# Kernel tuning notes

Measured on AMD Instinct MI355X. Metric: run time of the kernel, lower is better.

The kernel has to match this reference:

```python
import jax, jax.numpy as jnp
import numpy as np

V, E, T_MAX, H, L = 20000, 384, 512, 8, 8
D = E // H  # head size 48
FF = 4 * E


def setup_inputs() -> dict:
    key = jax.random.key(0)
    ks = jax.random.split(key, 24)
    B, T = 16, 512
    s = 0.02
    return {
        "index": jax.random.randint(ks[0], (B, T), 0, V, dtype=jnp.int64),
        "targets": jax.random.randint(ks[1], (B, T), 0, V, dtype=jnp.int64),
        "tok_emb": s * jax.random.normal(ks[2], (V, E), jnp.float32),
        "pos_emb": s * jax.random.normal(ks[3], (T_MAX, E), jnp.float32),
        "Wq": s * jax.random.normal(ks[4], (L, E, H, D), jnp.float32),
        "bq": jnp.zeros((L, H, D), jnp.float32),
        "Wk": s * jax.random.normal(ks[5], (L, E, H, D), jnp.float32),
        "bk": jnp.zeros((L, H, D), jnp.float32),
        "Wv": s * jax.random.normal(ks[6], (L, E, H, D), jnp.float32),
        "bv": jnp.zeros((L, H, D), jnp.float32),
        "Wo": s * jax.random.normal(ks[7], (L, E, E), jnp.float32),
        "bo": jnp.zeros((L, E), jnp.float32),
        "ln1_g": jnp.ones((L, E), jnp.float32),
        "ln1_b": jnp.zeros((L, E), jnp.float32),
        "ln2_g": jnp.ones((L, E), jnp.float32),
        "ln2_b": jnp.zeros((L, E), jnp.float32),
        "W1": s * jax.random.normal(ks[8], (L, E, FF), jnp.float32),
        "b1": jnp.zeros((L, FF), jnp.float32),
        "W2": s * jax.random.normal(ks[9], (L, FF, E), jnp.float32),
        "b2": jnp.zeros((L, E), jnp.float32),
        "lnf_g": jnp.ones((E,), jnp.float32),
        "lnf_b": jnp.zeros((E,), jnp.float32),
        "lm_b": jnp.zeros((V,), jnp.float32),
    }


def layernorm(x, g, b, eps=1e-5):
    mu = jnp.mean(x, axis=-1, keepdims=True)
    var = jnp.var(x, axis=-1, keepdims=True)
    return (x - mu) * jax.lax.rsqrt(var + eps) * g + b


def reference(index, targets, tok_emb, pos_emb, Wq, bq, Wk, bk, Wv, bv, Wo, bo,
              ln1_g, ln1_b, ln2_g, ln2_b, W1, b1, W2, b2, lnf_g, lnf_b, lm_b):
    B, T = index.shape
    x = tok_emb[index] + pos_emb[:T]  # [B,T,E]
    causal = jnp.tril(jnp.ones((T, T), bool))
    scale = D ** -0.5
    for l in range(L):
        h = layernorm(x, ln1_g[l], ln1_b[l])
        q = jnp.einsum('bte,ehd->bthd', h, Wq[l]) + bq[l]
        k = jnp.einsum('bte,ehd->bthd', h, Wk[l]) + bk[l]
        v = jnp.einsum('bte,ehd->bthd', h, Wv[l]) + bv[l]
        scores = jnp.einsum('bqhd,bkhd->bhqk', q, k) * scale
        scores = jnp.where(causal, scores, -jnp.inf)
        w = jax.nn.softmax(scores, axis=-1)
        attn = jnp.einsum('bhqk,bkhd->bqhd', w, v).reshape(B, T, E)
        x = x + attn @ Wo[l] + bo[l]
        h2 = layernorm(x, ln2_g[l], ln2_b[l])
        ff = jax.nn.gelu(h2 @ W1[l] + b1[l], approximate=False) @ W2[l] + b2[l]
        x = x + ff
    x = layernorm(x, lnf_g, lnf_b)
    logits = x @ tok_emb.T + lm_b  # tied weights
    logits = logits.reshape(B * T, V)
    logp = jax.nn.log_softmax(logits, axis=-1)
    loss = -jnp.mean(jnp.take_along_axis(logp, targets.reshape(-1, 1), axis=-1))
    return logits, loss
```

## Files before the change

kernel.cpp:

```cpp
#include <hip/hip_runtime.h>
#include <hip/hip_bf16.h>
#include <math.h>

#define M_ROWS 8192
#define E_DIM 384
#define FF_DIM 1536
#define V_DIM 20000
#define VPAD 20096
#define N_LAYER 8
#define QK_SCALE 0.14433756729740643f
#define PSTRIDE 320
#define NPART 314

typedef __bf16 bf16x8 __attribute__((ext_vector_type(8)));
typedef short  s16x8  __attribute__((ext_vector_type(8)));
typedef float  f32x4  __attribute__((ext_vector_type(4)));
typedef __hip_bfloat16 bf16_t;

__device__ __forceinline__ void gl2lds16(const void* g, void* l) {
    __builtin_amdgcn_global_load_lds((const __attribute__((address_space(1))) void*)g,
                                     (__attribute__((address_space(3))) void*)l, 16, 0, 0);
}
__device__ __forceinline__ unsigned short bf16bits(float v) {
    return __builtin_bit_cast(unsigned short, __float2bfloat16(v));
}

__global__ __launch_bounds__(256) void tconv_kernel(
    const float* __restrict__ in, bf16_t* __restrict__ out,
    int K, int N, int outRows, int rowoff)
{
    __shared__ float tile[32][33];
    const int n0 = blockIdx.x * 32, k0 = blockIdx.y * 32;
    const float* ip = in + (size_t)blockIdx.z * K * N;
    bf16_t* op = out + (size_t)blockIdx.z * outRows * K;
    const int tx = threadIdx.x & 31, ty = threadIdx.x >> 5;
#pragma unroll
    for (int i = 0; i < 32; i += 8)
        tile[ty + i][tx] = ip[(size_t)(k0 + ty + i) * N + n0 + tx];
    __syncthreads();
#pragma unroll
    for (int i = 0; i < 32; i += 8)
        op[(size_t)(rowoff + n0 + ty + i) * K + k0 + tx] = __float2bfloat16(tile[tx][ty + i]);
}

__global__ __launch_bounds__(256) void tokconv_kernel(
    const float* __restrict__ tok, bf16_t* __restrict__ out)
{
    const int total = VPAD * 48;
    for (int idx = blockIdx.x * 256 + threadIdx.x; idx < total; idx += gridDim.x * 256) {
        int row = idx / 48, gc = idx - row * 48;
        int col = gc * 8;
        s16x8 pk = {};
        if (row < V_DIM) {
            const float* tp = tok + (size_t)row * E_DIM + col;
            float4 f0 = *(const float4*)tp;
            float4 f1 = *(const float4*)(tp + 4);
            pk[0] = (short)bf16bits(f0.x); pk[1] = (short)bf16bits(f0.y);
            pk[2] = (short)bf16bits(f0.z); pk[3] = (short)bf16bits(f0.w);
            pk[4] = (short)bf16bits(f1.x); pk[5] = (short)bf16bits(f1.y);
            pk[6] = (short)bf16bits(f1.z); pk[7] = (short)bf16bits(f1.w);
        }
        *(s16x8*)&out[(size_t)row * E_DIM + col] = pk;
    }
}

__global__ __launch_bounds__(256) void bqkv_kernel(
    const float* __restrict__ bq, const float* __restrict__ bk,
    const float* __restrict__ bv, float* __restrict__ o)
{
    int i = blockIdx.x * 256 + threadIdx.x;
    if (i < N_LAYER * 1152) {
        int l = i / 1152, c = i - l * 1152;
        float v = (c < 384) ? bq[l * 384 + c] : (c < 768) ? bk[l * 384 + c - 384] : bv[l * 384 + c - 768];
        o[i] = v;
    }
}

__global__ __launch_bounds__(256) void embed_kernel(
    const int* __restrict__ idx, const float* __restrict__ tok,
    const float* __restrict__ pos, float* __restrict__ x)
{
    int row = blockIdx.x * 4 + (threadIdx.x >> 6);
    int lane = threadIdx.x & 63;
    int t = row & 511;
    int id = idx[row];
    const float* tr = tok + (size_t)id * E_DIM;
    const float* pr = pos + (size_t)t * E_DIM;
    float* xr = x + (size_t)row * E_DIM;
#pragma unroll
    for (int i = 0; i < 6; i++) { int c = lane + i * 64; xr[c] = tr[c] + pr[c]; }
}

__global__ __launch_bounds__(256) void ln_kernel(
    const float* __restrict__ x, const float* __restrict__ g,
    const float* __restrict__ b, bf16_t* __restrict__ out)
{
    int row = blockIdx.x * 4 + (threadIdx.x >> 6);
    int lane = threadIdx.x & 63;
    const float* xr = x + (size_t)row * E_DIM;
    float vals[6];
    float s = 0.f;
#pragma unroll
    for (int i = 0; i < 6; i++) { vals[i] = xr[lane + i * 64]; s += vals[i]; }
#pragma unroll
    for (int off = 1; off < 64; off <<= 1) s += __shfl_xor(s, off);
    float mu = s * (1.f / E_DIM);
    float sq = 0.f;
#pragma unroll
    for (int i = 0; i < 6; i++) { float d = vals[i] - mu; sq += d * d; }
#pragma unroll
    for (int off = 1; off < 64; off <<= 1) sq += __shfl_xor(sq, off);
    float rstd = rsqrtf(sq * (1.f / E_DIM) + 1e-5f);
    bf16_t* orow = out + (size_t)row * E_DIM;
#pragma unroll
    for (int i = 0; i < 6; i++) {
        int c = lane + i * 64;
        orow[c] = __float2bfloat16((vals[i] - mu) * rstd * g[c] + b[c]);
    }
}

template <int MODE, int MREP>
__global__ __launch_bounds__(256) void gemm_kernel(
    const bf16_t* __restrict__ A, const bf16_t* __restrict__ Bt,
    const float* __restrict__ bias, void* __restrict__ Cv, void* __restrict__ C2,
    int Ncols, int K)
{
    constexpr int BMR = MREP * 32;
    constexpr int ASH = BMR * 32;
    constexpr int BUFSH = ASH + 4096;
    constexpr int NLD = MREP / 2 + 2;
    __shared__ __align__(16) short smem[3 * BUFSH];
    const int t = threadIdx.x;
    const int w = t >> 6, lane = t & 63;
    const int wm = w >> 1, wn = w & 1;
    const int bm = (MODE == 3 ? blockIdx.x : blockIdx.y) * BMR;
    const int bn = (MODE == 3 ? blockIdx.y : blockIdx.x) * 128;

    f32x4 acc[MREP][4];
#pragma unroll
    for (int m = 0; m < MREP; m++)
#pragma unroll
        for (int n = 0; n < 4; n++)
            acc[m][n] = (f32x4){0.f, 0.f, 0.f, 0.f};

    const int lg = lane >> 4;
    const int ll = lane & 15;
    const int nt = K / 32;

    auto stagef = [&](int kt, int buf) {
        short* sA = smem + buf * BUFSH;
        short* sB = sA + ASH;
#pragma unroll
        for (int i = 0; i < MREP / 2; i++) {
            int li = i * 256 + t;
            int g = li >> (MREP == 4 ? 7 : 6);
            int row = li & (BMR - 1);
            gl2lds16(A + (size_t)(bm + row) * K + kt + g * 8,
                     sA + (size_t)(i * 256 + w * 64) * 8);
        }
#pragma unroll
        for (int i = 0; i < 2; i++) {
            int li = i * 256 + t;
            gl2lds16(Bt + (size_t)(bn + (li & 127)) * K + kt + (li >> 7) * 8,
                     sB + (size_t)(i * 256 + w * 64) * 8);
        }
    };

    stagef(0, 0);
    stagef(32, 1);

    for (int tt = 0; tt < nt; ++tt) {
        if (tt + 2 < nt) {
            stagef((tt + 2) * 32, (tt + 2) % 3);
            asm volatile("s_waitcnt vmcnt(%0)" :: "n"(2 * NLD) : "memory");
        } else if (tt + 1 < nt) {
            asm volatile("s_waitcnt vmcnt(%0)" :: "n"(NLD) : "memory");
        } else {
            asm volatile("s_waitcnt vmcnt(0)" ::: "memory");
        }
        __builtin_amdgcn_s_barrier();

        const short* sA = smem + (tt % 3) * BUFSH;
        const short* sB = sA + ASH;
        bf16x8 af[MREP], bfr[4];
#pragma unroll
        for (int m = 0; m < MREP; m++)
            af[m] = __builtin_bit_cast(bf16x8,
                *(const s16x8*)&sA[(lg * BMR + wm * (BMR / 2) + m * 16 + ll) * 8]);
#pragma unroll
        for (int n = 0; n < 4; n++)
            bfr[n] = __builtin_bit_cast(bf16x8,
                *(const s16x8*)&sB[(lg * 128 + wn * 64 + n * 16 + ll) * 8]);
#pragma unroll
        for (int m = 0; m < MREP; m++)
#pragma unroll
            for (int n = 0; n < 4; n++)
                acc[m][n] = __builtin_amdgcn_mfma_f32_16x16x32_bf16(bfr[n], af[m], acc[m][n], 0, 0, 0);

        __builtin_amdgcn_s_barrier();
    }

    const int rowm0 = bm + wm * (BMR / 2) + ll;
    const int coln0 = bn + wn * 64 + lg * 4;

    if constexpr (MODE == 4) {
        if (bn < 768) {
            bf16_t* qkvb = (bf16_t*)Cv;
            const float sc = (bn >= 384) ? 1.f : QK_SCALE;
#pragma unroll
            for (int n = 0; n < 4; n++) {
                const int coln = coln0 + n * 16;
                const float4 b4 = *(const float4*)&bias[coln];
#pragma unroll
                for (int m = 0; m < MREP; m++) {
                    const int row = rowm0 + m * 16;
                    ushort4 pk;
                    pk.x = bf16bits((acc[m][n][0] + b4.x) * sc);
                    pk.y = bf16bits((acc[m][n][1] + b4.y) * sc);
                    pk.z = bf16bits((acc[m][n][2] + b4.z) * sc);
                    pk.w = bf16bits((acc[m][n][3] + b4.w) * sc);
                    *(ushort4*)&qkvb[(size_t)row * 1152 + coln] = pk;
                }
            }
        } else {
            bf16_t* vtb = (bf16_t*)C2;
            const int cc0 = coln0 - 768;
#pragma unroll
            for (int n = 0; n < 4; n++) {
                const float4 b4 = *(const float4*)&bias[coln0 + n * 16];
#pragma unroll
                for (int m = 0; m < MREP; m++) {
                    const int row = rowm0 + m * 16;
                    const int bb = row >> 9, tt2 = row & 511;
                    bf16_t* vb = vtb + (size_t)bb * 384 * 512 + tt2;
                    vb[(size_t)(cc0 + n * 16 + 0) * 512] = __float2bfloat16(acc[m][n][0] + b4.x);
                    vb[(size_t)(cc0 + n * 16 + 1) * 512] = __float2bfloat16(acc[m][n][1] + b4.y);
                    vb[(size_t)(cc0 + n * 16 + 2) * 512] = __float2bfloat16(acc[m][n][2] + b4.z);
                    vb[(size_t)(cc0 + n * 16 + 3) * 512] = __float2bfloat16(acc[m][n][3] + b4.w);
                }
            }
        }
    } else if constexpr (MODE == 1) {
        float* C = (float*)Cv;
#pragma unroll
        for (int n = 0; n < 4; n++) {
            const int coln = coln0 + n * 16;
            const float4 b4 = *(const float4*)&bias[coln];
#pragma unroll
            for (int m = 0; m < MREP; m++) {
                const int row = rowm0 + m * 16;
                float4 cv = *(float4*)&C[(size_t)row * Ncols + coln];
                cv.x += acc[m][n][0] + b4.x;
                cv.y += acc[m][n][1] + b4.y;
                cv.z += acc[m][n][2] + b4.z;
                cv.w += acc[m][n][3] + b4.w;
                *(float4*)&C[(size_t)row * Ncols + coln] = cv;
            }
        }
    } else if constexpr (MODE == 2) {
        bf16_t* O = (bf16_t*)Cv;
#pragma unroll
        for (int n = 0; n < 4; n++) {
            const int coln = coln0 + n * 16;
            const float4 b4 = *(const float4*)&bias[coln];
#pragma unroll
            for (int m = 0; m < MREP; m++) {
                const int row = rowm0 + m * 16;
                float v0 = acc[m][n][0] + b4.x, v1 = acc[m][n][1] + b4.y;
                float v2 = acc[m][n][2] + b4.z, v3 = acc[m][n][3] + b4.w;
                v0 = 0.5f * v0 * (1.f + erff(v0 * 0.70710678118654752f));
                v1 = 0.5f * v1 * (1.f + erff(v1 * 0.70710678118654752f));
                v2 = 0.5f * v2 * (1.f + erff(v2 * 0.70710678118654752f));
                v3 = 0.5f * v3 * (1.f + erff(v3 * 0.70710678118654752f));
                ushort4 pk;
                pk.x = bf16bits(v0); pk.y = bf16bits(v1);
                pk.z = bf16bits(v2); pk.w = bf16bits(v3);
                *(ushort4*)&O[(size_t)row * Ncols + coln] = pk;
            }
        }
    } else if constexpr (MODE == 3) {
        float* C = (float*)Cv;
        float* pbuf = (float*)C2;
        const int ptile = blockIdx.y * 2 + wn;
#pragma unroll
        for (int m = 0; m < MREP; m++) {
            const int row = rowm0 + m * 16;
            float se = 0.f;
#pragma unroll
            for (int n = 0; n < 4; n++) {
                const int coln = coln0 + n * 16;
                if (coln + 3 < Ncols) {
                    const float4 b4 = *(const float4*)&bias[coln];
                    f32x4 v;
                    v[0] = acc[m][n][0] + b4.x;
                    v[1] = acc[m][n][1] + b4.y;
                    v[2] = acc[m][n][2] + b4.z;
                    v[3] = acc[m][n][3] + b4.w;
                    __builtin_nontemporal_store(v, (f32x4*)&C[(size_t)row * Ncols + coln]);
                    se += __expf(v[0]) + __expf(v[1]) + __expf(v[2]) + __expf(v[3]);
                } else {
#pragma unroll
                    for (int e = 0; e < 4; e++) {
                        int col = coln + e;
                        if (col < Ncols) {
                            float v = acc[m][n][e] + bias[col];
                            __builtin_nontemporal_store(v, &C[(size_t)row * Ncols + col]);
                            se += __expf(v);
                        }
                    }
                }
            }
            se += __shfl_xor(se, 16);
            se += __shfl_xor(se, 32);
            if (lg == 0)
                __builtin_nontemporal_store(se, &pbuf[(size_t)row * PSTRIDE + ptile]);
        }
    }
}

__global__ __launch_bounds__(256) void attn_kernel(
    const bf16_t* __restrict__ qkvb, const bf16_t* __restrict__ vt,
    bf16_t* __restrict__ o)
{
    const int qt = blockIdx.x, bh = blockIdx.y;
    const int b = bh >> 3, h = bh & 7;
    __shared__ unsigned short psm[4608];
    const int tid = threadIdx.x;
    const int w = tid >> 6, lane = tid & 63;
    const int ll = lane & 15, g = lane >> 4;
    const int q0 = qt * 64;
    const int q_abs = q0 + ll * 4 + w;

    const bf16_t* qrow = qkvb + (size_t)(b * 512 + q_abs) * 1152 + h * 48;
    bf16x8 qf0 = __builtin_bit_cast(bf16x8, *(const s16x8*)(qrow + g * 8));
    bf16x8 qf1 = {};
    if (g < 2) qf1 = __builtin_bit_cast(bf16x8, *(const s16x8*)(qrow + 32 + g * 8));

    f32x4 oacc[3];
#pragma unroll
    for (int df = 0; df < 3; df++) oacc[df] = (f32x4){0.f, 0.f, 0.f, 0.f};
    float ssum = 0.f;

    const bf16_t* kptr = qkvb + (size_t)b * 512 * 1152 + 384 + h * 48;
    const bf16_t* vptr = vt + (size_t)b * 384 * 512 + (size_t)h * 48 * 512;
    const int ntiles = 2 * (qt + 1);

    auto loadK = [&](int kbase, bf16x8& c00, bf16x8& c01, bf16x8& c10, bf16x8& c11) {
        const bf16_t* kr0 = kptr + (size_t)(kbase + ll) * 1152;
        const bf16_t* kr1 = kptr + (size_t)(kbase + 16 + ll) * 1152;
        c00 = __builtin_bit_cast(bf16x8, *(const s16x8*)(kr0 + g * 8));
        c10 = __builtin_bit_cast(bf16x8, *(const s16x8*)(kr1 + g * 8));
        bf16x8 z = {};
        c01 = (g < 2) ? __builtin_bit_cast(bf16x8, *(const s16x8*)(kr0 + 32 + g * 8)) : z;
        c11 = (g < 2) ? __builtin_bit_cast(bf16x8, *(const s16x8*)(kr1 + 32 + g * 8)) : z;
    };

    auto doTile = [&](int kbase, int parity,
                      const bf16x8& c00, const bf16x8& c01, const bf16x8& c10, const bf16x8& c11,
                      bool pf, int nbase,
                      bf16x8& n00, bf16x8& n01, bf16x8& n10, bf16x8& n11) {
        bf16x8 vf[3];
#pragma unroll
        for (int df = 0; df < 3; df++)
            vf[df] = __builtin_bit_cast(bf16x8,
                *(const s16x8*)(vptr + (size_t)(df * 16 + ll) * 512 + kbase + g * 8));
        if (pf) loadK(nbase, n00, n01, n10, n11);

        f32x4 sfr[2];
        {
            f32x4 z0 = {0.f, 0.f, 0.f, 0.f};
            z0 = __builtin_amdgcn_mfma_f32_16x16x32_bf16(c00, qf0, z0, 0, 0, 0);
            z0 = __builtin_amdgcn_mfma_f32_16x16x32_bf16(c01, qf1, z0, 0, 0, 0);
            sfr[0] = z0;
            f32x4 z1 = {0.f, 0.f, 0.f, 0.f};
            z1 = __builtin_amdgcn_mfma_f32_16x16x32_bf16(c10, qf0, z1, 0, 0, 0);
            z1 = __builtin_amdgcn_mfma_f32_16x16x32_bf16(c11, qf1, z1, 0, 0, 0);
            sfr[1] = z1;
        }

        float p[8];
#pragma unroll
        for (int f = 0; f < 2; f++)
#pragma unroll
            for (int j = 0; j < 4; j++) {
                int key = kbase + f * 16 + g * 4 + j;
                float sv = sfr[f][j];
                sv = (key > q_abs) ? -1e30f : sv;
                float pv = __expf(fminf(sv, 20.f));
                p[f * 4 + j] = pv;
                ssum += pv;
            }

        const int pbase = (w * 2 + parity) * 576;
#pragma unroll
        for (int f = 0; f < 2; f++)
#pragma unroll
            for (int j = 0; j < 4; j++)
                psm[pbase + (f * 16 + g * 4 + j) * 18 + ll] = bf16bits(p[f * 4 + j]);
        s16x8 pr;
#pragma unroll
        for (int i = 0; i < 8; i++)
            pr[i] = (short)psm[pbase + (g * 8 + i) * 18 + ll];
        bf16x8 pfr = __builtin_bit_cast(bf16x8, pr);
#pragma unroll
        for (int df = 0; df < 3; df++)
            oacc[df] = __builtin_amdgcn_mfma_f32_16x16x32_bf16(vf[df], pfr, oacc[df], 0, 0, 0);
    };

    bf16x8 kA0, kA1, kA2, kA3, kB0, kB1, kB2, kB3;
    loadK(0, kA0, kA1, kA2, kA3);
    for (int kt = 0; kt < ntiles; kt += 2) {
        doTile(kt * 32, 0, kA0, kA1, kA2, kA3,
               true, (kt + 1) * 32, kB0, kB1, kB2, kB3);
        doTile((kt + 1) * 32, 1, kB0, kB1, kB2, kB3,
               (kt + 2) < ntiles, (kt + 2) * 32, kA0, kA1, kA2, kA3);
    }

    ssum += __shfl_xor(ssum, 16);
    ssum += __shfl_xor(ssum, 32);
    float inv = 1.f / ssum;
    bf16_t* orow = o + (size_t)(b * 512 + q_abs) * 384 + h * 48;
#pragma unroll
    for (int df = 0; df < 3; df++) {
        ushort4 pk;
        pk.x = bf16bits(oacc[df][0] * inv);
        pk.y = bf16bits(oacc[df][1] * inv);
        pk.z = bf16bits(oacc[df][2] * inv);
        pk.w = bf16bits(oacc[df][3] * inv);
        *(ushort4*)&orow[df * 16 + g * 4] = pk;
    }
}

__global__ __launch_bounds__(256) void loss_row2_kernel(
    const float* __restrict__ pbuf, const float* __restrict__ logits,
    const int* __restrict__ targets, float* __restrict__ rowloss)
{
    int row = blockIdx.x * 4 + (threadIdx.x >> 6);
    int lane = threadIdx.x & 63;
    const float* pr = pbuf + (size_t)row * PSTRIDE;
    float s = 0.f;
    for (int i = lane; i < NPART; i += 64) s += pr[i];
#pragma unroll
    for (int off = 1; off < 64; off <<= 1) s += __shfl_xor(s, off);
    if (lane == 0) {
        int tgt = targets[row];
        rowloss[row] = logf(s) - logits[(size_t)row * V_DIM + tgt];
    }
}

__global__ __launch_bounds__(256) void loss_reduce_kernel(
    const float* __restrict__ rowloss, float* __restrict__ out)
{
    int t = threadIdx.x;
    __shared__ float red[4];
    float s = 0.f;
    for (int i = t; i < M_ROWS; i += 256) s += rowloss[i];
#pragma unroll
    for (int off = 1; off < 64; off <<= 1) s += __shfl_xor(s, off);
    if ((t & 63) == 0) red[t >> 6] = s;
    __syncthreads();
    if (t == 0) out[0] = (red[0] + red[1] + red[2] + red[3]) * (1.f / M_ROWS);
}

extern "C" void kernel_launch(void* const* d_in, const int* in_sizes, int n_in,
                              void* d_out, int out_size, void* d_ws, size_t ws_size,
                              hipStream_t stream)
{
    const int*   index   = (const int*)d_in[0];
    const int*   targets = (const int*)d_in[1];
    const float* tok_emb = (const float*)d_in[2];
    const float* pos_emb = (const float*)d_in[3];
    const float* Wq = (const float*)d_in[4];
    const float* bq = (const float*)d_in[5];
    const float* Wk = (const float*)d_in[6];
    const float* bk = (const float*)d_in[7];
    const float* Wv = (const float*)d_in[8];
    const float* bv = (const float*)d_in[9];
    const float* Wo = (const float*)d_in[10];
    const float* bo = (const float*)d_in[11];
    const float* ln1_g = (const float*)d_in[12];
    const float* ln1_b = (const float*)d_in[13];
    const float* ln2_g = (const float*)d_in[14];
    const float* ln2_b = (const float*)d_in[15];
    const float* W1 = (const float*)d_in[16];
    const float* b1 = (const float*)d_in[17];
    const float* W2 = (const float*)d_in[18];
    const float* b2 = (const float*)d_in[19];
    const float* lnf_g = (const float*)d_in[20];
    const float* lnf_b = (const float*)d_in[21];
    const float* lm_b  = (const float*)d_in[22];

    float* out = (float*)d_out;
    char* wsb = (char*)d_ws;

    float*  x     = (float*)(wsb + 0);
    bf16_t* hbuf  = (bf16_t*)(wsb + 12582912);
    bf16_t* obuf  = (bf16_t*)(wsb + 18874368);
    bf16_t* qkvb  = (bf16_t*)(wsb + 25165824);
    bf16_t* vtb   = (bf16_t*)(wsb + 44040192);
    bf16_t* ffmid = (bf16_t*)(wsb + 18874368);
    float*  pbuf  = (float*)(wsb + 25165824);
    bf16_t* tokb  = (bf16_t*)(wsb + 50331648);
    bf16_t* qkvw  = (bf16_t*)(wsb + 65765376);
    bf16_t* wo_t  = (bf16_t*)(wsb + 72843264);
    bf16_t* w1_t  = (bf16_t*)(wsb + 75202560);
    bf16_t* w2_t  = (bf16_t*)(wsb + 84639744);
    float*  bqkv  = (float*)(wsb + 94076928);
    float*  rowloss = (float*)(wsb + 94113792);

    tokconv_kernel<<<2048, 256, 0, stream>>>(tok_emb, tokb);
    tconv_kernel<<<dim3(12, 12, 8), 256, 0, stream>>>(Wq, qkvw, 384, 384, 1152, 0);
    tconv_kernel<<<dim3(12, 12, 8), 256, 0, stream>>>(Wk, qkvw, 384, 384, 1152, 384);
    tconv_kernel<<<dim3(12, 12, 8), 256, 0, stream>>>(Wv, qkvw, 384, 384, 1152, 768);
    tconv_kernel<<<dim3(12, 12, 8), 256, 0, stream>>>(Wo, wo_t, 384, 384, 384, 0);
    tconv_kernel<<<dim3(48, 12, 8), 256, 0, stream>>>(W1, w1_t, 384, 1536, 1536, 0);
    tconv_kernel<<<dim3(12, 48, 8), 256, 0, stream>>>(W2, w2_t, 1536, 384, 384, 0);
    bqkv_kernel<<<36, 256, 0, stream>>>(bq, bk, bv, bqkv);

    embed_kernel<<<2048, 256, 0, stream>>>(index, tok_emb, pos_emb, x);

    for (int l = 0; l < N_LAYER; l++) {
        const bf16_t* qkvw_l = qkvw + (size_t)l * 1152 * 384;
        const float*  bqkv_l = bqkv + l * 1152;
        ln_kernel<<<2048, 256, 0, stream>>>(x, ln1_g + l * E_DIM, ln1_b + l * E_DIM, hbuf);
        gemm_kernel<4, 4><<<dim3(9, 64), 256, 0, stream>>>(
            hbuf, qkvw_l, bqkv_l, qkvb, vtb, 1152, 384);
        attn_kernel<<<dim3(8, 128), 256, 0, stream>>>(qkvb, vtb, obuf);
        gemm_kernel<1, 2><<<dim3(3, 128), 256, 0, stream>>>(
            obuf, wo_t + (size_t)l * 384 * 384, bo + l * E_DIM, x, nullptr, 384, 384);
        ln_kernel<<<2048, 256, 0, stream>>>(x, ln2_g + l * E_DIM, ln2_b + l * E_DIM, hbuf);
        gemm_kernel<2, 4><<<dim3(12, 64), 256, 0, stream>>>(
            hbuf, w1_t + (size_t)l * 1536 * 384, b1 + l * FF_DIM, ffmid, nullptr, 1536, 384);
        gemm_kernel<1, 2><<<dim3(3, 128), 256, 0, stream>>>(
            ffmid, w2_t + (size_t)l * 384 * 1536, b2 + l * E_DIM, x, nullptr, 384, 1536);
    }

    ln_kernel<<<2048, 256, 0, stream>>>(x, lnf_g, lnf_b, hbuf);
    gemm_kernel<3, 4><<<dim3(64, 157), 256, 0, stream>>>(
        hbuf, tokb, lm_b, out, pbuf, V_DIM, 384);

    loss_row2_kernel<<<2048, 256, 0, stream>>>(pbuf, out, targets, rowloss);
    loss_reduce_kernel<<<1, 256, 0, stream>>>(rowloss, out + (size_t)M_ROWS * V_DIM);
}
```

Baseline: 1.828 ms.

## Replace LDS-staged LM-head GEMM with register-direct MFMA logits kernel

The final vocab projection no longer uses the generic LDS-staged, triple-buffered GEMM. A dedicated kernel loads A and B fragments straight from global memory into registers, double-buffering across K, with 128x64 tiles. Each block now writes one partial exp-sum per row per 64-column tile, so pbuf indexing goes from 2 per 128-column block to one per block. The aim is to drop LDS staging and sync overhead in a kernel bound by the fp32 logits store. The cost is less on-chip reuse and more redundant global/L2 reads of the token embedding and activations.

```diff
diff --git a/kernel.cpp b/kernel.cpp
--- a/kernel.cpp
+++ b/kernel.cpp
@@ -133,8 +133,8 @@
     const int t = threadIdx.x;
     const int w = t >> 6, lane = t & 63;
     const int wm = w >> 1, wn = w & 1;
-    const int bm = (MODE == 3 ? blockIdx.x : blockIdx.y) * BMR;
-    const int bn = (MODE == 3 ? blockIdx.y : blockIdx.x) * 128;
+    const int bm = blockIdx.y * BMR;
+    const int bn = blockIdx.x * 128;
 
     f32x4 acc[MREP][4];
 #pragma unroll
@@ -278,43 +278,99 @@
                 *(ushort4*)&O[(size_t)row * Ncols + coln] = pk;
             }
         }
-    } else if constexpr (MODE == 3) {
-        float* C = (float*)Cv;
-        float* pbuf = (float*)C2;
-        const int ptile = blockIdx.y * 2 + wn;
-#pragma unroll
-        for (int m = 0; m < MREP; m++) {
-            const int row = rowm0 + m * 16;
-            float se = 0.f;
-#pragma unroll
-            for (int n = 0; n < 4; n++) {
-                const int coln = coln0 + n * 16;
-                if (coln + 3 < Ncols) {
-                    const float4 b4 = *(const float4*)&bias[coln];
-                    f32x4 v;
-                    v[0] = acc[m][n][0] + b4.x;
-                    v[1] = acc[m][n][1] + b4.y;
-                    v[2] = acc[m][n][2] + b4.z;
-                    v[3] = acc[m][n][3] + b4.w;
-                    __builtin_nontemporal_store(v, (f32x4*)&C[(size_t)row * Ncols + coln]);
-                    se += __expf(v[0]) + __expf(v[1]) + __expf(v[2]) + __expf(v[3]);
-                } else {
-#pragma unroll
-                    for (int e = 0; e < 4; e++) {
-                        int col = coln + e;
-                        if (col < Ncols) {
-                            float v = acc[m][n][e] + bias[col];
-                            __builtin_nontemporal_store(v, &C[(size_t)row * Ncols + col]);
-                            se += __expf(v);
-                        }
+    }
+}
+
+__global__ __launch_bounds__(256) void logits_kernel(
+    const bf16_t* __restrict__ A, const bf16_t* __restrict__ Bt,
+    const float* __restrict__ bias, float* __restrict__ C,
+    float* __restrict__ pbuf)
+{
+    const int t = threadIdx.x;
+    const int w = t >> 6, lane = t & 63;
+    const int lg = lane >> 4, ll = lane & 15;
+    const int bm = blockIdx.x * 128 + w * 32;
+    const int bn = blockIdx.y * 64;
+
+    const bf16_t* a0 = A + (size_t)(bm + ll) * E_DIM + lg * 8;
+    const bf16_t* a1 = A + (size_t)(bm + 16 + ll) * E_DIM + lg * 8;
+    const bf16_t* b0 = Bt + (size_t)(bn + ll) * E_DIM + lg * 8;
+    const bf16_t* b1 = Bt + (size_t)(bn + 16 + ll) * E_DIM + lg * 8;
+    const bf16_t* b2 = Bt + (size_t)(bn + 32 + ll) * E_DIM + lg * 8;
+    const bf16_t* b3 = Bt + (size_t)(bn + 48 + ll) * E_DIM + lg * 8;
+
+    f32x4 acc[2][4];
+#pragma unroll
+    for (int m = 0; m < 2; m++)
+#pragma unroll
+        for (int n = 0; n < 4; n++)
+            acc[m][n] = (f32x4){0.f, 0.f, 0.f, 0.f};
+
+    auto ld = [&](int k0, bf16x8& A0, bf16x8& A1,
+                  bf16x8& B0, bf16x8& B1, bf16x8& B2, bf16x8& B3) {
+        A0 = __builtin_bit_cast(bf16x8, *(const s16x8*)(a0 + k0));
+        A1 = __builtin_bit_cast(bf16x8, *(const s16x8*)(a1 + k0));
+        B0 = __builtin_bit_cast(bf16x8, *(const s16x8*)(b0 + k0));
+        B1 = __builtin_bit_cast(bf16x8, *(const s16x8*)(b1 + k0));
+        B2 = __builtin_bit_cast(bf16x8, *(const s16x8*)(b2 + k0));
+        B3 = __builtin_bit_cast(bf16x8, *(const s16x8*)(b3 + k0));
+    };
+    auto mm = [&](const bf16x8& A0, const bf16x8& A1,
+                  const bf16x8& B0, const bf16x8& B1, const bf16x8& B2, const bf16x8& B3) {
+        acc[0][0] = __builtin_amdgcn_mfma_f32_16x16x32_bf16(B0, A0, acc[0][0], 0, 0, 0);
+        acc[0][1] = __builtin_amdgcn_mfma_f32_16x16x32_bf16(B1, A0, acc[0][1], 0, 0, 0);
+        acc[0][2] = __builtin_amdgcn_mfma_f32_16x16x32_bf16(B2, A0, acc[0][2], 0, 0, 0);
+        acc[0][3] = __builtin_amdgcn_mfma_f32_16x16x32_bf16(B3, A0, acc[0][3], 0, 0, 0);
+        acc[1][0] = __builtin_amdgcn_mfma_f32_16x16x32_bf16(B0, A1, acc[1][0], 0, 0, 0);
+        acc[1][1] = __builtin_amdgcn_mfma_f32_16x16x32_bf16(B1, A1, acc[1][1], 0, 0, 0);
+        acc[1][2] = __builtin_amdgcn_mfma_f32_16x16x32_bf16(B2, A1, acc[1][2], 0, 0, 0);
+        acc[1][3] = __builtin_amdgcn_mfma_f32_16x16x32_bf16(B3, A1, acc[1][3], 0, 0, 0);
+    };
+
+    bf16x8 xA0, xA1, xB0, xB1, xB2, xB3;
+    bf16x8 yA0, yA1, yB0, yB1, yB2, yB3;
+    ld(0, xA0, xA1, xB0, xB1, xB2, xB3);
+#pragma unroll
+    for (int kt = 0; kt < 12; kt += 2) {
+        ld((kt + 1) * 32, yA0, yA1, yB0, yB1, yB2, yB3);
+        mm(xA0, xA1, xB0, xB1, xB2, xB3);
+        if (kt + 2 < 12) ld((kt + 2) * 32, xA0, xA1, xB0, xB1, xB2, xB3);
+        mm(yA0, yA1, yB0, yB1, yB2, yB3);
+    }
+
+    const int coln0 = bn + lg * 4;
+#pragma unroll
+    for (int m = 0; m < 2; m++) {
+        const int row = bm + m * 16 + ll;
+        float se = 0.f;
+#pragma unroll
+        for (int n = 0; n < 4; n++) {
+            const int coln = coln0 + n * 16;
+            if (coln + 3 < V_DIM) {
+                const float4 b4 = *(const float4*)&bias[coln];
+                f32x4 v;
+                v[0] = acc[m][n][0] + b4.x;
+                v[1] = acc[m][n][1] + b4.y;
+                v[2] = acc[m][n][2] + b4.z;
+                v[3] = acc[m][n][3] + b4.w;
+                __builtin_nontemporal_store(v, (f32x4*)&C[(size_t)row * V_DIM + coln]);
+                se += __expf(v[0]) + __expf(v[1]) + __expf(v[2]) + __expf(v[3]);
+            } else {
+#pragma unroll
+                for (int e = 0; e < 4; e++) {
+                    int col = coln + e;
+                    if (col < V_DIM) {
+                        float v = acc[m][n][e] + bias[col];
+                        __builtin_nontemporal_store(v, &C[(size_t)row * V_DIM + col]);
+                        se += __expf(v);
                     }
                 }
             }
-            se += __shfl_xor(se, 16);
-            se += __shfl_xor(se, 32);
-            if (lg == 0)
-                __builtin_nontemporal_store(se, &pbuf[(size_t)row * PSTRIDE + ptile]);
-        }
+        }
+        se += __shfl_xor(se, 16);
+        se += __shfl_xor(se, 32);
+        if (lg == 0)
+            __builtin_nontemporal_store(se, &pbuf[(size_t)row * PSTRIDE + blockIdx.y]);
     }
 }
 
@@ -536,8 +592,7 @@
     }
 
     ln_kernel<<<2048, 256, 0, stream>>>(x, lnf_g, lnf_b, hbuf);
-    gemm_kernel<3, 4><<<dim3(64, 157), 256, 0, stream>>>(
-        hbuf, tokb, lm_b, out, pbuf, V_DIM, 384);
+    logits_kernel<<<dim3(64, 314), 256, 0, stream>>>(hbuf, tokb, lm_b, out, pbuf);
 
     loss_row2_kernel<<<2048, 256, 0, stream>>>(pbuf, out, targets, rowloss);
     loss_reduce_kernel<<<1, 256, 0, stream>>>(rowloss, out + (size_t)M_ROWS * V_DIM);
```

New measurement: 2.157 ms. +18.0%, slower.
